# Performance work log

Measured on AMD Instinct MI355X. Metric: run time of the kernel, lower is better.

## Reference

```python
import jax, jax.numpy as jnp
import numpy as np

B, N, R, E = 4, 50000, 100000, 1_600_000   # batch, nodes (wavelets_col), wavelets_row, nnz
D_IN, H1, H2, D_OUT = 32, 32, 16, 1
NEG_SLOPE = 0.2


def _xavier(k, shape):
    lim = float(np.sqrt(6.0 / (shape[0] + shape[1])))
    return jax.random.uniform(k, shape, jnp.float32, -lim, lim)


def setup_inputs() -> dict:
    key = jax.random.key(0)
    ks = jax.random.split(key, 16)
    # wavelets: sparse (R x N); inverse wavelets: sparse (N x R)
    w_rows = jax.random.randint(ks[0], (E,), 0, R)
    w_cols = jax.random.randint(ks[1], (E,), 0, N)
    wi_rows = jax.random.randint(ks[2], (E,), 0, N)
    wi_cols = jax.random.randint(ks[3], (E,), 0, R)
    return {
        "wavelets_indices": jnp.stack([w_rows, w_cols]),
        "wavelets_values": jax.random.normal(ks[4], (E,), jnp.float32) * 0.05,
        "wavelets_inverse_indices": jnp.stack([wi_rows, wi_cols]),
        "wavelets_inverse_values": jax.random.normal(ks[5], (E,), jnp.float32) * 0.05,
        "x_features": jax.random.normal(ks[6], (B, N, D_IN), jnp.float32),
        "W1": _xavier(ks[7], (D_IN, H1)),
        "diag1": 0.9 + 0.2 * jax.random.uniform(ks[8], (R,), jnp.float32),
        "W2": _xavier(ks[9], (H1, H2)),
        "diag2": 0.9 + 0.2 * jax.random.uniform(ks[10], (R,), jnp.float32),
        "reg_co_w": _xavier(ks[11], (H2, D_OUT)),
        "reg_co_b": jnp.zeros((D_OUT,), jnp.float32),
        "reg_co2_w": _xavier(ks[12], (H2, D_OUT)),
        "reg_co2_b": jnp.zeros((D_OUT,), jnp.float32),
    }


def _gw_layer(x, W, diag, w_idx, w_val, wi_idx, wi_val):
    # filtered = X @ W  -> (B, N, d)
    h = jnp.einsum("bnd,de->bne", x, W)
    d = W.shape[1]
    # T = wavelets (R x N) @ h  : scatter-add of gathered edge messages
    msg = h[:, w_idx[1], :] * w_val[None, :, None]          # (B, E, d)
    t = jnp.zeros((x.shape[0], R, d), h.dtype).at[:, w_idx[0], :].add(msg)
    # out = (wavelets_inverse * diag) (N x R) @ T  (diag rescales columns)
    coef = wi_val * diag[wi_idx[1]]                         # (E,)
    msg2 = t[:, wi_idx[1], :] * coef[None, :, None]         # (B, E, d)
    out = jnp.zeros((x.shape[0], N, d), h.dtype).at[:, wi_idx[0], :].add(msg2)
    return jax.nn.leaky_relu(out, NEG_SLOPE)                # dropout p=0.0 -> identity


def reference(wavelets_indices, wavelets_values, wavelets_inverse_indices,
              wavelets_inverse_values, x_features, W1, diag1, W2, diag2,
              reg_co_w, reg_co_b, reg_co2_w, reg_co2_b):
    x = _gw_layer(x_features, W1, diag1, wavelets_indices, wavelets_values,
                  wavelets_inverse_indices, wavelets_inverse_values)
    x = _gw_layer(x, W2, diag2, wavelets_indices, wavelets_values,
                  wavelets_inverse_indices, wavelets_inverse_values)
    co = x[:, -2, :] @ reg_co_w + reg_co_b                  # (B, 1)
    co2 = x[:, -1, :] @ reg_co2_w + reg_co2_b               # (B, 1)
    return jnp.concatenate([co[:, None, :], co2[:, None, :]], axis=1)  # (B, 2, 1)
```

## Files before the change

### kernel.cpp

```cpp
#include <hip/hip_runtime.h>

#define NEG_SLOPE 0.2f

static const int B = 4, N = 50000, R = 100000, E = 1600000;
static const int X2_CAP = 4096;
static const int R2_CAP = 4096;
static const int N1_CAP = 4096;
static const int WDEG  = 64;
static const int WIDEG = 96;
static const int RBW = 3200;
static const int NBW = 1600;


__global__ void fusedA(const float* __restrict__ x, const float* __restrict__ W1,
                       float* __restrict__ h1,
                       const int4* __restrict__ wi_rows4, const int* __restrict__ wi_cols,
                       const float* __restrict__ wi_val,
                       unsigned* __restrict__ bitsR1, int2* __restrict__ x2list,
                       int* __restrict__ x2tail, int* __restrict__ r2list,
                       int* __restrict__ r2tail, int e4, int G1) {
    if ((int)blockIdx.x < G1) {
        __shared__ float sW[32 * 32];
        for (int i = threadIdx.x; i < 1024; i += blockDim.x) sW[i] = W1[i];
        __syncthreads();
        int id = blockIdx.x * blockDim.x + threadIdx.x;
        if (id >= N * B) return;
        int n = id >> 2, b = id & 3;
        const float* xr = x + ((size_t)b * N + n) * 32;
        float acc[32];
#pragma unroll
        for (int c = 0; c < 32; ++c) acc[c] = 0.f;
#pragma unroll
        for (int k = 0; k < 32; ++k) {
            float xv = xr[k];
#pragma unroll
            for (int c = 0; c < 32; ++c) acc[c] += xv * sW[k * 32 + c];
        }
        float* o = h1 + ((size_t)n * B + b) * 32;
#pragma unroll
        for (int c = 0; c < 32; ++c) o[c] = acc[c];
    } else {
        int blk = blockIdx.x - G1;
        int base = blk * (blockDim.x * 4) + threadIdx.x;
#pragma unroll
        for (int k = 0; k < 4; ++k) {
            int i = base + k * blockDim.x;
            if (i >= e4) continue;
            int4 r = wi_rows4[i];
            int rr[4] = {r.x, r.y, r.z, r.w};
#pragma unroll
            for (int j = 0; j < 4; ++j) {
                if (rr[j] >= N - 2) {
                    int ed = i * 4 + j;
                    int col = wi_cols[ed];
                    unsigned old = atomicOr(&bitsR1[col >> 5], 1u << (col & 31));
                    if (!((old >> (col & 31)) & 1u)) {
                        int p = atomicAdd(r2tail, 1);
                        if (p < R2_CAP) r2list[p] = col;
                    }
                    int pos = atomicAdd(x2tail, 1);
                    if (pos < X2_CAP)
                        x2list[pos] = make_int2(col * 2 + (rr[j] - (N - 2)),
                                                __float_as_int(wi_val[ed]));
                }
            }
        }
    }
}

__global__ void markB(const int4* __restrict__ w_rows4, const int* __restrict__ w_cols,
                      const unsigned* __restrict__ bitsR1, unsigned* __restrict__ bitsN1,
                      int* __restrict__ n1list, int* __restrict__ n1slot,
                      int* __restrict__ n1tail, int e4) {
    __shared__ int lcount, gbase;
    __shared__ int sbuf[1024];
    if (threadIdx.x == 0) lcount = 0;
    __syncthreads();
    int lane = threadIdx.x & 63;
    int i = blockIdx.x * blockDim.x + threadIdx.x;
    int4 r = make_int4(-1, -1, -1, -1);
    if (i < e4) r = w_rows4[i];
    int rr[4] = {r.x, r.y, r.z, r.w};
    unsigned fb[4];
#pragma unroll
    for (int j = 0; j < 4; ++j)
        fb[j] = (rr[j] >= 0) ? ((bitsR1[rr[j] >> 5] >> (rr[j] & 31)) & 1u) : 0u;
#pragma unroll
    for (int j = 0; j < 4; ++j) {
        bool isnew = false;
        int c = 0;
        if (fb[j]) {
            c = w_cols[i * 4 + j];
            unsigned old = atomicOr(&bitsN1[c >> 5], 1u << (c & 31));
            isnew = ((old >> (c & 31)) & 1u) == 0u;
        }
        unsigned long long m = __ballot(isnew);
        if (m) {
            int leader = __ffsll(m) - 1;
            int b0 = 0;
            if (lane == leader) b0 = atomicAdd(&lcount, __popcll(m));
            b0 = __shfl(b0, leader);
            if (isnew) sbuf[b0 + __popcll(m & ((1ull << lane) - 1))] = c;
        }
    }
    __syncthreads();
    if (threadIdx.x == 0) gbase = atomicAdd(n1tail, lcount);
    __syncthreads();
    for (int t = threadIdx.x; t < lcount; t += blockDim.x) {
        int n = sbuf[t];
        int slot = gbase + t;
        n1list[slot] = n;
        n1slot[n] = slot;
    }
}

__global__ void markC_wi(const int4* __restrict__ wi_rows4, const int* __restrict__ wi_cols,
                         const float* __restrict__ wi_val, const float* __restrict__ diag1,
                         const unsigned* __restrict__ bitsN1, const int* __restrict__ n1slot,
                         unsigned* __restrict__ bitsR2, int* __restrict__ wi_cnt,
                         int2* __restrict__ wi_pairsD,
                         int* __restrict__ r1list, int* __restrict__ r1tail, int e4) {
    __shared__ int lcount2, gbase2;
    __shared__ int r1buf[1024];
    if (threadIdx.x == 0) lcount2 = 0;
    __syncthreads();
    int lane = threadIdx.x & 63;
    int i = blockIdx.x * blockDim.x + threadIdx.x;
    int4 r = make_int4(-1, -1, -1, -1);
    if (i < e4) r = wi_rows4[i];
    int rr[4] = {r.x, r.y, r.z, r.w};
    unsigned fb[4];
#pragma unroll
    for (int j = 0; j < 4; ++j)
        fb[j] = (rr[j] >= 0) ? ((bitsN1[rr[j] >> 5] >> (rr[j] & 31)) & 1u) : 0u;
#pragma unroll
    for (int j = 0; j < 4; ++j) {
        bool isnew = false;
        int col = 0;
        if (fb[j]) {
            int ed = i * 4 + j;
            col = wi_cols[ed];
            float cf = wi_val[ed] * diag1[col];
            int slot = n1slot[rr[j]];
            int pos = atomicAdd(&wi_cnt[rr[j]], 1);
            if (slot < N1_CAP && pos < WIDEG)
                wi_pairsD[(size_t)slot * WIDEG + pos] =
                    make_int2(col, __float_as_int(cf));
            unsigned old = atomicOr(&bitsR2[col >> 5], 1u << (col & 31));
            isnew = ((old >> (col & 31)) & 1u) == 0u;
        }
        unsigned long long m2 = __ballot(isnew);
        if (m2) {
            int leader = __ffsll(m2) - 1;
            int b0 = 0;
            if (lane == leader) b0 = atomicAdd(&lcount2, __popcll(m2));
            b0 = __shfl(b0, leader);
            if (isnew)
                r1buf[b0 + __popcll(m2 & ((1ull << lane) - 1))] = col;
        }
    }
    __syncthreads();
    if (threadIdx.x == 0) gbase2 = atomicAdd(r1tail, lcount2);
    __syncthreads();
    for (int t = threadIdx.x; t < lcount2; t += blockDim.x) r1list[gbase2 + t] = r1buf[t];
}

__global__ void wplace(const int4* __restrict__ w_rows4, const int4* __restrict__ w_cols4,
                       const float4* __restrict__ w_val4,
                       const unsigned* __restrict__ bitsR1, const unsigned* __restrict__ bitsR2,
                       int* __restrict__ w_cnt, int2* __restrict__ w_pairsD, int e4) {
    int i = blockIdx.x * blockDim.x + threadIdx.x;
    if (i >= e4) return;
    int4 r = w_rows4[i];
    int4 c = w_cols4[i];
    float4 v = w_val4[i];
    int rr[4] = {r.x, r.y, r.z, r.w};
    int cc[4] = {c.x, c.y, c.z, c.w};
    float vv[4] = {v.x, v.y, v.z, v.w};
    unsigned fl[4];
#pragma unroll
    for (int j = 0; j < 4; ++j)
        fl[j] = ((bitsR1[rr[j] >> 5] | bitsR2[rr[j] >> 5]) >> (rr[j] & 31)) & 1u;
#pragma unroll
    for (int j = 0; j < 4; ++j) {
        if (fl[j]) {
            int pos = atomicAdd(&w_cnt[rr[j]], 1);
            if (pos < WDEG)
                w_pairsD[(size_t)rr[j] * WDEG + pos] =
                    make_int2(cc[j], __float_as_int(vv[j]));
        }
    }
}

__global__ void gather_t1(const float* __restrict__ h1, float* __restrict__ t1,
                          const int* __restrict__ w_cnt, const int2* __restrict__ w_pairsD,
                          const int* __restrict__ r1list, const int* __restrict__ r1tail) {
    int total = (*r1tail) * 32;
    int gstride = gridDim.x * blockDim.x;
    for (int idx = blockIdx.x * blockDim.x + threadIdx.x; idx < total; idx += gstride) {
        int row = r1list[idx >> 5];
        int rem = idx & 31;
        int c4 = rem & 7;
        int b = rem >> 3;
        int L = w_cnt[row]; if (L > WDEG) L = WDEG;
        const int2* pr = w_pairsD + (size_t)row * WDEG;
        const float4* sb = (const float4*)h1 + b * 8 + c4;
        float4 acc = make_float4(0.f, 0.f, 0.f, 0.f);
        int i = 0;
        int L4 = L & ~3;
        for (; i < L4; i += 4) {
            int2 p0 = pr[i + 0];
            int2 p1 = pr[i + 1];
            int2 p2 = pr[i + 2];
            int2 p3 = pr[i + 3];
            float4 s0 = sb[(size_t)p0.x * 32];
            float4 s1 = sb[(size_t)p1.x * 32];
            float4 s2 = sb[(size_t)p2.x * 32];
            float4 s3 = sb[(size_t)p3.x * 32];
            float v0 = __int_as_float(p0.y), v1 = __int_as_float(p1.y);
            float v2 = __int_as_float(p2.y), v3 = __int_as_float(p3.y);
            acc.x += v0 * s0.x + v1 * s1.x + v2 * s2.x + v3 * s3.x;
            acc.y += v0 * s0.y + v1 * s1.y + v2 * s2.y + v3 * s3.y;
            acc.z += v0 * s0.z + v1 * s1.z + v2 * s2.z + v3 * s3.z;
            acc.w += v0 * s0.w + v1 * s1.w + v2 * s2.w + v3 * s3.w;
        }
        for (; i < L; ++i) {
            int2 p = pr[i];
            float4 sv = sb[(size_t)p.x * 32];
            float v = __int_as_float(p.y);
            acc.x += v * sv.x; acc.y += v * sv.y; acc.z += v * sv.z; acc.w += v * sv.w;
        }
        ((float4*)t1)[(size_t)row * 32 + b * 8 + c4] = acc;
    }
}

__global__ void x1gemm2(const float* __restrict__ t1, const float* __restrict__ W2,
                        float* __restrict__ h2,
                        const int* __restrict__ n1list, const int* __restrict__ wi_cnt,
                        const int2* __restrict__ wi_pairsD,
                        const int* __restrict__ n1tail) {
    __shared__ float sW[32 * 16];
    __shared__ float xls[8][128];
    for (int i = threadIdx.x; i < 512; i += blockDim.x) sW[i] = W2[i];
    int n1c = *n1tail; if (n1c > N1_CAP) n1c = N1_CAP;
    int g = threadIdx.x >> 5;
    int t32 = threadIdx.x & 31;
    int b = t32 >> 3, c4 = t32 & 7;
    for (int base = blockIdx.x * 8; base < n1c; base += gridDim.x * 8) {
        int s = base + g;
        bool active = (s < n1c);
        int n = 0;
        if (active) {
            n = n1list[s];
            int L = wi_cnt[n]; if (L > WIDEG) L = WIDEG;
            const int2* pr = wi_pairsD + (size_t)s * WIDEG;
            const float4* sb = (const float4*)t1 + b * 8 + c4;
            float4 acc = make_float4(0.f, 0.f, 0.f, 0.f);
            int i = 0;
            int L2 = L & ~1;
            for (; i < L2; i += 2) {
                int2 p0 = pr[i + 0];
                int2 p1 = pr[i + 1];
                float4 s0 = sb[(size_t)p0.x * 32];
                float4 s1 = sb[(size_t)p1.x * 32];
                float v0 = __int_as_float(p0.y), v1 = __int_as_float(p1.y);
                acc.x += v0 * s0.x + v1 * s1.x;
                acc.y += v0 * s0.y + v1 * s1.y;
                acc.z += v0 * s0.z + v1 * s1.z;
                acc.w += v0 * s0.w + v1 * s1.w;
            }
            if (i < L) {
                int2 p = pr[i];
                float4 sv = sb[(size_t)p.x * 32];
                float v = __int_as_float(p.y);
                acc.x += v * sv.x; acc.y += v * sv.y; acc.z += v * sv.z; acc.w += v * sv.w;
            }
            float* xp = &xls[g][b * 32 + c4 * 4];
            xp[0] = acc.x > 0.f ? acc.x : NEG_SLOPE * acc.x;
            xp[1] = acc.y > 0.f ? acc.y : NEG_SLOPE * acc.y;
            xp[2] = acc.z > 0.f ? acc.z : NEG_SLOPE * acc.z;
            xp[3] = acc.w > 0.f ? acc.w : NEG_SLOPE * acc.w;
        }
        __syncthreads();
        if (active) {
#pragma unroll
            for (int half = 0; half < 2; ++half) {
                int o = t32 + half * 32;
                int bb = o >> 4, cc = o & 15;
                const float* xp = &xls[g][bb * 32];
                float acc = 0.f;
#pragma unroll
                for (int k = 0; k < 32; ++k) acc += xp[k] * sW[k * 16 + cc];
                h2[(size_t)n * 64 + o] = acc;
            }
        }
        __syncthreads();
    }
}

__global__ void t2x2heads(const float* __restrict__ h2,
                          const int* __restrict__ w_cnt, const int2* __restrict__ w_pairsD,
                          const int* __restrict__ r2list, const int* __restrict__ r2tail,
                          float* __restrict__ t2,
                          const int2* __restrict__ x2list, const int* __restrict__ x2tail,
                          const float* __restrict__ diag2,
                          const float* __restrict__ rw1, const float* __restrict__ rb1,
                          const float* __restrict__ rw2, const float* __restrict__ rb2,
                          float* __restrict__ out) {
    int r2c = *r2tail; if (r2c > R2_CAP) r2c = R2_CAP;
    for (int idx = threadIdx.x; idx < r2c * 16; idx += blockDim.x) {
        int row = r2list[idx >> 4];
        int rem = idx & 15;
        int c4 = rem & 3;
        int b = rem >> 2;
        int L = w_cnt[row]; if (L > WDEG) L = WDEG;
        const int2* pr = w_pairsD + (size_t)row * WDEG;
        const float4* sb = (const float4*)h2 + b * 4 + c4;
        float4 acc = make_float4(0.f, 0.f, 0.f, 0.f);
        for (int i = 0; i < L; ++i) {
            int2 p = pr[i];
            float4 sv = sb[(size_t)p.x * 16];
            float v = __int_as_float(p.y);
            acc.x += v * sv.x; acc.y += v * sv.y; acc.z += v * sv.z; acc.w += v * sv.w;
        }
        ((float4*)t2)[(size_t)row * 16 + b * 4 + c4] = acc;
    }
    __syncthreads();

    int cnt = *x2tail; if (cnt > X2_CAP) cnt = X2_CAP;
    int g = threadIdx.x >> 6, l = threadIdx.x & 63;
    int b = l >> 4, c = l & 15;
    float a0 = 0.f, a1 = 0.f;
    for (int i = g; i < cnt; i += 16) {
        int2 rec = x2list[i];
        int col = rec.x >> 1;
        float coef = __int_as_float(rec.y) * diag2[col];
        float v = t2[(size_t)col * 64 + b * 16 + c] * coef;
        if (rec.x & 1) a1 += v; else a0 += v;
    }
    __shared__ float red0[16][64], red1[16][64], xs[2][64];
    red0[g][l] = a0; red1[g][l] = a1;
    __syncthreads();
    if (threadIdx.x < 64) {
        float s0 = 0.f, s1 = 0.f;
#pragma unroll
        for (int gg = 0; gg < 16; ++gg) { s0 += red0[gg][l]; s1 += red1[gg][l]; }
        xs[0][l] = s0; xs[1][l] = s1;
    }
    __syncthreads();
    if (threadIdx.x < 8) {
        int bb = threadIdx.x >> 1, which = threadIdx.x & 1;
        const float* w = which ? rw2 : rw1;
        float acc = which ? rb2[0] : rb1[0];
        for (int k = 0; k < 16; ++k) {
            float xv = xs[which][bb * 16 + k];
            xv = xv > 0.f ? xv : NEG_SLOPE * xv;
            acc += xv * w[k];
        }
        out[bb * 2 + which] = acc;
    }
}

extern "C" void kernel_launch(void* const* d_in, const int* in_sizes, int n_in,
                              void* d_out, int out_size, void* d_ws, size_t ws_size,
                              hipStream_t stream) {
    const int*   w_rows  = (const int*)d_in[0];
    const int*   w_cols  = ((const int*)d_in[0]) + E;
    const float* w_val   = (const float*)d_in[1];
    const int*   wi_rows = (const int*)d_in[2];
    const int*   wi_cols = ((const int*)d_in[2]) + E;
    const float* wi_val  = (const float*)d_in[3];
    const float* x       = (const float*)d_in[4];
    const float* W1      = (const float*)d_in[5];
    const float* diag1   = (const float*)d_in[6];
    const float* W2      = (const float*)d_in[7];
    const float* diag2   = (const float*)d_in[8];
    const float* rw1     = (const float*)d_in[9];
    const float* rb1     = (const float*)d_in[10];
    const float* rw2     = (const float*)d_in[11];
    const float* rb2     = (const float*)d_in[12];
    float* out = (float*)d_out;

    float* h1 = (float*)d_ws;
    float* t1 = h1 + (size_t)B * N * 32;
    float* h2 = t1 + (size_t)B * R * 32;
    int* ip = (int*)(h2 + (size_t)B * N * 16);
    int* w_cnt  = ip; ip += R;
    int* wi_cnt = ip; ip += N;
    unsigned* bitsR1 = (unsigned*)ip; ip += RBW;
    unsigned* bitsR2 = (unsigned*)ip; ip += RBW;
    unsigned* bitsN1 = (unsigned*)ip; ip += NBW;
    int* tails  = ip; ip += 8;
    size_t zero_words = (size_t)(ip - w_cnt);
    int*  n1slot = ip; ip += N;
    int*  n1list = ip; ip += N;
    int*  r1list = ip; ip += R;
    int*  r2list = ip; ip += R2_CAP;
    int2* x2list = (int2*)ip; ip += 2 * X2_CAP;
    int2* w_pairsD  = (int2*)ip; ip += 2 * (size_t)R * WDEG;
    int2* wi_pairsD = (int2*)ip; ip += 2 * (size_t)N1_CAP * WIDEG;

    float* t2 = t1;

    const int blk = 256;
    const int e4 = E / 4;
    const int G1 = (N * B + blk - 1) / blk;
    const int G2 = (e4 + blk * 4 - 1) / (blk * 4);
    const int scanGrid = (e4 + blk - 1) / blk;

    (void)hipMemsetAsync(w_cnt, 0, zero_words * sizeof(int), stream);

    fusedA<<<G1 + G2, blk, 0, stream>>>(x, W1, h1, (const int4*)wi_rows, wi_cols, wi_val,
                                        bitsR1, x2list, tails + 0, r2list, tails + 1,
                                        e4, G1);
    markB<<<scanGrid, blk, 0, stream>>>((const int4*)w_rows, w_cols, bitsR1, bitsN1,
                                        n1list, n1slot, tails + 2, e4);
    markC_wi<<<scanGrid, blk, 0, stream>>>((const int4*)wi_rows, wi_cols, wi_val, diag1,
                                           bitsN1, n1slot, bitsR2, wi_cnt, wi_pairsD,
                                           r1list, tails + 3, e4);
    wplace<<<scanGrid, blk, 0, stream>>>((const int4*)w_rows, (const int4*)w_cols,
                                         (const float4*)w_val, bitsR1, bitsR2,
                                         w_cnt, w_pairsD, e4);
    gather_t1<<<4096, blk, 0, stream>>>(h1, t1, w_cnt, w_pairsD, r1list, tails + 3);
    x1gemm2<<<256, blk, 0, stream>>>(t1, W2, h2, n1list, wi_cnt, wi_pairsD, tails + 2);
    t2x2heads<<<1, 1024, 0, stream>>>(h2, w_cnt, w_pairsD, r2list, tails + 1,
                                      t2, x2list, tails + 0, diag2,
                                      rw1, rb1, rw2, rb2, out);
}
```

Measured before the change: 278.1 us.

## Fuse all phases into one cooperative persistent kernel with grid syncs

Replaces the memset and seven separate kernel launches with a single cooperative kernel that zeroes the workspace, then runs each marking, placement, gather and head phase separated by grid-wide syncs. The intent is to remove launch gaps and per-kernel ramp costs for a pipeline whose later phases touch only a small active subset. It also drops the full dense h1 = x@W1 product and fuses W1 into a later per-node stage, computing it only where needed. The cost is grid-sync overhead, fewer resident blocks looping over the edge arrays, and new 1024-entry per-block buffer caps that silently drop entries on overflow.

```diff
diff --git a/kernel.cpp b/kernel.cpp
--- a/kernel.cpp
+++ b/kernel.cpp
@@ -1,4 +1,7 @@
 #include <hip/hip_runtime.h>
+#include <hip/hip_cooperative_groups.h>
+
+namespace cg = cooperative_groups;
 
 #define NEG_SLOPE 0.2f
 
@@ -10,420 +13,421 @@
 static const int WIDEG = 96;
 static const int RBW = 3200;
 static const int NBW = 1600;
-
-
-__global__ void fusedA(const float* __restrict__ x, const float* __restrict__ W1,
-                       float* __restrict__ h1,
-                       const int4* __restrict__ wi_rows4, const int* __restrict__ wi_cols,
-                       const float* __restrict__ wi_val,
-                       unsigned* __restrict__ bitsR1, int2* __restrict__ x2list,
-                       int* __restrict__ x2tail, int* __restrict__ r2list,
-                       int* __restrict__ r2tail, int e4, int G1) {
-    if ((int)blockIdx.x < G1) {
-        __shared__ float sW[32 * 32];
-        for (int i = threadIdx.x; i < 1024; i += blockDim.x) sW[i] = W1[i];
+static const int ZWORDS = R + N + RBW + RBW + NBW + 8;
+
+struct KParams {
+    const int4*  w_rows4;  const int* w_cols;  const float* w_val;
+    const int4*  wi_rows4; const int* wi_cols; const float* wi_val;
+    const float* x;  const float* W1; const float* diag1;
+    const float* W2; const float* diag2;
+    const float* rw1; const float* rb1; const float* rw2; const float* rb2;
+    float* out;
+    float* t1;
+    float* h2;
+    int* w_cnt; int* wi_cnt;
+    unsigned* bitsR1; unsigned* bitsR2; unsigned* bitsN1;
+    int* tails;
+    int* n1slot; int* n1list; int* r1list; int* r2list;
+    int2* x2list; int2* w_pairsD; int2* wi_pairsD;
+    int e4;
+};
+
+union SMem {
+    struct { int lcount; int gbase; int buf[1024]; } comp;
+    struct { float W1s[1024]; float W2s[512];
+             float uls[8][128]; float x1ls[8][128]; } p6;
+    struct { float red0[4][64]; float red1[4][64]; float xs[2][64]; } p8;
+};
+
+__global__ void __launch_bounds__(256, 4) fused(KParams P) {
+    cg::grid_group grid = cg::this_grid();
+    const int tid  = threadIdx.x;
+    const int gtid = blockIdx.x * blockDim.x + tid;
+    const int T    = gridDim.x * blockDim.x;
+    const int lane = tid & 63;
+    __shared__ SMem sm;
+
+    for (int i = gtid; i < ZWORDS; i += T) P.w_cnt[i] = 0;
+    grid.sync();
+
+    for (int i = gtid; i < P.e4; i += T) {
+        int4 r = P.wi_rows4[i];
+        int rr[4] = {r.x, r.y, r.z, r.w};
+#pragma unroll
+        for (int j = 0; j < 4; ++j) {
+            if (rr[j] >= N - 2) {
+                int ed = i * 4 + j;
+                int col = P.wi_cols[ed];
+                unsigned old = atomicOr(&P.bitsR1[col >> 5], 1u << (col & 31));
+                if (!((old >> (col & 31)) & 1u)) {
+                    int p = atomicAdd(&P.tails[1], 1);
+                    if (p < R2_CAP) P.r2list[p] = col;
+                }
+                int pos = atomicAdd(&P.tails[0], 1);
+                if (pos < X2_CAP)
+                    P.x2list[pos] = make_int2(col * 2 + (rr[j] - (N - 2)),
+                                              __float_as_int(P.wi_val[ed]));
+            }
+        }
+    }
+    grid.sync();
+
+    if (tid == 0) sm.comp.lcount = 0;
+    __syncthreads();
+    {
+        int niter = (P.e4 + T - 1) / T;
+        for (int it = 0; it < niter; ++it) {
+            int i = it * T + gtid;
+            int4 r = make_int4(-1, -1, -1, -1);
+            if (i < P.e4) r = P.w_rows4[i];
+            int rr[4] = {r.x, r.y, r.z, r.w};
+            unsigned fb[4];
+#pragma unroll
+            for (int j = 0; j < 4; ++j)
+                fb[j] = (rr[j] >= 0) ? ((P.bitsR1[rr[j] >> 5] >> (rr[j] & 31)) & 1u) : 0u;
+#pragma unroll
+            for (int j = 0; j < 4; ++j) {
+                bool isnew = false;
+                int c = 0;
+                if (fb[j]) {
+                    c = P.w_cols[i * 4 + j];
+                    unsigned old = atomicOr(&P.bitsN1[c >> 5], 1u << (c & 31));
+                    isnew = ((old >> (c & 31)) & 1u) == 0u;
+                }
+                unsigned long long m = __ballot(isnew);
+                if (m) {
+                    int leader = __ffsll(m) - 1;
+                    int b0 = 0;
+                    if (lane == leader) b0 = atomicAdd(&sm.comp.lcount, __popcll(m));
+                    b0 = __shfl(b0, leader);
+                    if (isnew) {
+                        int p = b0 + __popcll(m & ((1ull << lane) - 1));
+                        if (p < 1024) sm.comp.buf[p] = c;
+                    }
+                }
+            }
+        }
+    }
+    __syncthreads();
+    {
+        int lc = sm.comp.lcount; if (lc > 1024) lc = 1024;
+        if (tid == 0) sm.comp.gbase = atomicAdd(&P.tails[2], lc);
         __syncthreads();
-        int id = blockIdx.x * blockDim.x + threadIdx.x;
-        if (id >= N * B) return;
-        int n = id >> 2, b = id & 3;
-        const float* xr = x + ((size_t)b * N + n) * 32;
-        float acc[32];
-#pragma unroll
-        for (int c = 0; c < 32; ++c) acc[c] = 0.f;
-#pragma unroll
-        for (int k = 0; k < 32; ++k) {
-            float xv = xr[k];
-#pragma unroll
-            for (int c = 0; c < 32; ++c) acc[c] += xv * sW[k * 32 + c];
-        }
-        float* o = h1 + ((size_t)n * B + b) * 32;
-#pragma unroll
-        for (int c = 0; c < 32; ++c) o[c] = acc[c];
-    } else {
-        int blk = blockIdx.x - G1;
-        int base = blk * (blockDim.x * 4) + threadIdx.x;
-#pragma unroll
-        for (int k = 0; k < 4; ++k) {
-            int i = base + k * blockDim.x;
-            if (i >= e4) continue;
-            int4 r = wi_rows4[i];
+        for (int t = tid; t < lc; t += 256) {
+            int n = sm.comp.buf[t];
+            int slot = sm.comp.gbase + t;
+            if (slot < N1_CAP) { P.n1list[slot] = n; P.n1slot[n] = slot; }
+        }
+    }
+    grid.sync();
+
+    if (tid == 0) sm.comp.lcount = 0;
+    __syncthreads();
+    {
+        int niter = (P.e4 + T - 1) / T;
+        for (int it = 0; it < niter; ++it) {
+            int i = it * T + gtid;
+            int4 r = make_int4(-1, -1, -1, -1);
+            if (i < P.e4) r = P.wi_rows4[i];
             int rr[4] = {r.x, r.y, r.z, r.w};
+            unsigned fb[4];
+#pragma unroll
+            for (int j = 0; j < 4; ++j)
+                fb[j] = (rr[j] >= 0) ? ((P.bitsN1[rr[j] >> 5] >> (rr[j] & 31)) & 1u) : 0u;
 #pragma unroll
             for (int j = 0; j < 4; ++j) {
-                if (rr[j] >= N - 2) {
+                bool isnew = false;
+                int col = 0;
+                if (fb[j]) {
                     int ed = i * 4 + j;
-                    int col = wi_cols[ed];
-                    unsigned old = atomicOr(&bitsR1[col >> 5], 1u << (col & 31));
-                    if (!((old >> (col & 31)) & 1u)) {
-                        int p = atomicAdd(r2tail, 1);
-                        if (p < R2_CAP) r2list[p] = col;
+                    col = P.wi_cols[ed];
+                    float cf = P.wi_val[ed] * P.diag1[col];
+                    int slot = P.n1slot[rr[j]];
+                    int pos = atomicAdd(&P.wi_cnt[rr[j]], 1);
+                    if (slot < N1_CAP && pos < WIDEG)
+                        P.wi_pairsD[(size_t)slot * WIDEG + pos] =
+                            make_int2(col, __float_as_int(cf));
+                    unsigned old = atomicOr(&P.bitsR2[col >> 5], 1u << (col & 31));
+                    isnew = ((old >> (col & 31)) & 1u) == 0u;
+                }
+                unsigned long long m2 = __ballot(isnew);
+                if (m2) {
+                    int leader = __ffsll(m2) - 1;
+                    int b0 = 0;
+                    if (lane == leader) b0 = atomicAdd(&sm.comp.lcount, __popcll(m2));
+                    b0 = __shfl(b0, leader);
+                    if (isnew) {
+                        int p = b0 + __popcll(m2 & ((1ull << lane) - 1));
+                        if (p < 1024) sm.comp.buf[p] = col;
                     }
-                    int pos = atomicAdd(x2tail, 1);
-                    if (pos < X2_CAP)
-                        x2list[pos] = make_int2(col * 2 + (rr[j] - (N - 2)),
-                                                __float_as_int(wi_val[ed]));
-                }
-            }
-        }
-    }
-}
-
-__global__ void markB(const int4* __restrict__ w_rows4, const int* __restrict__ w_cols,
-                      const unsigned* __restrict__ bitsR1, unsigned* __restrict__ bitsN1,
-                      int* __restrict__ n1list, int* __restrict__ n1slot,
-                      int* __restrict__ n1tail, int e4) {
-    __shared__ int lcount, gbase;
-    __shared__ int sbuf[1024];
-    if (threadIdx.x == 0) lcount = 0;
+                }
+            }
+        }
+    }
     __syncthreads();
-    int lane = threadIdx.x & 63;
-    int i = blockIdx.x * blockDim.x + threadIdx.x;
-    int4 r = make_int4(-1, -1, -1, -1);
-    if (i < e4) r = w_rows4[i];
-    int rr[4] = {r.x, r.y, r.z, r.w};
-    unsigned fb[4];
-#pragma unroll
-    for (int j = 0; j < 4; ++j)
-        fb[j] = (rr[j] >= 0) ? ((bitsR1[rr[j] >> 5] >> (rr[j] & 31)) & 1u) : 0u;
-#pragma unroll
-    for (int j = 0; j < 4; ++j) {
-        bool isnew = false;
-        int c = 0;
-        if (fb[j]) {
-            c = w_cols[i * 4 + j];
-            unsigned old = atomicOr(&bitsN1[c >> 5], 1u << (c & 31));
-            isnew = ((old >> (c & 31)) & 1u) == 0u;
-        }
-        unsigned long long m = __ballot(isnew);
-        if (m) {
-            int leader = __ffsll(m) - 1;
-            int b0 = 0;
-            if (lane == leader) b0 = atomicAdd(&lcount, __popcll(m));
-            b0 = __shfl(b0, leader);
-            if (isnew) sbuf[b0 + __popcll(m & ((1ull << lane) - 1))] = c;
-        }
-    }
-    __syncthreads();
-    if (threadIdx.x == 0) gbase = atomicAdd(n1tail, lcount);
-    __syncthreads();
-    for (int t = threadIdx.x; t < lcount; t += blockDim.x) {
-        int n = sbuf[t];
-        int slot = gbase + t;
-        n1list[slot] = n;
-        n1slot[n] = slot;
-    }
-}
-
-__global__ void markC_wi(const int4* __restrict__ wi_rows4, const int* __restrict__ wi_cols,
-                         const float* __restrict__ wi_val, const float* __restrict__ diag1,
-                         const unsigned* __restrict__ bitsN1, const int* __restrict__ n1slot,
-                         unsigned* __restrict__ bitsR2, int* __restrict__ wi_cnt,
-                         int2* __restrict__ wi_pairsD,
-                         int* __restrict__ r1list, int* __restrict__ r1tail, int e4) {
-    __shared__ int lcount2, gbase2;
-    __shared__ int r1buf[1024];
-    if (threadIdx.x == 0) lcount2 = 0;
-    __syncthreads();
-    int lane = threadIdx.x & 63;
-    int i = blockIdx.x * blockDim.x + threadIdx.x;
-    int4 r = make_int4(-1, -1, -1, -1);
-    if (i < e4) r = wi_rows4[i];
-    int rr[4] = {r.x, r.y, r.z, r.w};
-    unsigned fb[4];
-#pragma unroll
-    for (int j = 0; j < 4; ++j)
-        fb[j] = (rr[j] >= 0) ? ((bitsN1[rr[j] >> 5] >> (rr[j] & 31)) & 1u) : 0u;
-#pragma unroll
-    for (int j = 0; j < 4; ++j) {
-        bool isnew = false;
-        int col = 0;
-        if (fb[j]) {
-            int ed = i * 4 + j;
-            col = wi_cols[ed];
-            float cf = wi_val[ed] * diag1[col];
-            int slot = n1slot[rr[j]];
-            int pos = atomicAdd(&wi_cnt[rr[j]], 1);
-            if (slot < N1_CAP && pos < WIDEG)
-                wi_pairsD[(size_t)slot * WIDEG + pos] =
-                    make_int2(col, __float_as_int(cf));
-            unsigned old = atomicOr(&bitsR2[col >> 5], 1u << (col & 31));
-            isnew = ((old >> (col & 31)) & 1u) == 0u;
-        }
-        unsigned long long m2 = __ballot(isnew);
-        if (m2) {
-            int leader = __ffsll(m2) - 1;
-            int b0 = 0;
-            if (lane == leader) b0 = atomicAdd(&lcount2, __popcll(m2));
-            b0 = __shfl(b0, leader);
-            if (isnew)
-                r1buf[b0 + __popcll(m2 & ((1ull << lane) - 1))] = col;
-        }
-    }
-    __syncthreads();
-    if (threadIdx.x == 0) gbase2 = atomicAdd(r1tail, lcount2);
-    __syncthreads();
-    for (int t = threadIdx.x; t < lcount2; t += blockDim.x) r1list[gbase2 + t] = r1buf[t];
-}
-
-__global__ void wplace(const int4* __restrict__ w_rows4, const int4* __restrict__ w_cols4,
-                       const float4* __restrict__ w_val4,
-                       const unsigned* __restrict__ bitsR1, const unsigned* __restrict__ bitsR2,
-                       int* __restrict__ w_cnt, int2* __restrict__ w_pairsD, int e4) {
-    int i = blockIdx.x * blockDim.x + threadIdx.x;
-    if (i >= e4) return;
-    int4 r = w_rows4[i];
-    int4 c = w_cols4[i];
-    float4 v = w_val4[i];
-    int rr[4] = {r.x, r.y, r.z, r.w};
-    int cc[4] = {c.x, c.y, c.z, c.w};
-    float vv[4] = {v.x, v.y, v.z, v.w};
-    unsigned fl[4];
-#pragma unroll
-    for (int j = 0; j < 4; ++j)
-        fl[j] = ((bitsR1[rr[j] >> 5] | bitsR2[rr[j] >> 5]) >> (rr[j] & 31)) & 1u;
-#pragma unroll
-    for (int j = 0; j < 4; ++j) {
-        if (fl[j]) {
-            int pos = atomicAdd(&w_cnt[rr[j]], 1);
-            if (pos < WDEG)
-                w_pairsD[(size_t)rr[j] * WDEG + pos] =
-                    make_int2(cc[j], __float_as_int(vv[j]));
-        }
-    }
-}
-
-__global__ void gather_t1(const float* __restrict__ h1, float* __restrict__ t1,
-                          const int* __restrict__ w_cnt, const int2* __restrict__ w_pairsD,
-                          const int* __restrict__ r1list, const int* __restrict__ r1tail) {
-    int total = (*r1tail) * 32;
-    int gstride = gridDim.x * blockDim.x;
-    for (int idx = blockIdx.x * blockDim.x + threadIdx.x; idx < total; idx += gstride) {
-        int row = r1list[idx >> 5];
-        int rem = idx & 31;
-        int c4 = rem & 7;
-        int b = rem >> 3;
-        int L = w_cnt[row]; if (L > WDEG) L = WDEG;
-        const int2* pr = w_pairsD + (size_t)row * WDEG;
-        const float4* sb = (const float4*)h1 + b * 8 + c4;
-        float4 acc = make_float4(0.f, 0.f, 0.f, 0.f);
-        int i = 0;
-        int L4 = L & ~3;
-        for (; i < L4; i += 4) {
-            int2 p0 = pr[i + 0];
-            int2 p1 = pr[i + 1];
-            int2 p2 = pr[i + 2];
-            int2 p3 = pr[i + 3];
-            float4 s0 = sb[(size_t)p0.x * 32];
-            float4 s1 = sb[(size_t)p1.x * 32];
-            float4 s2 = sb[(size_t)p2.x * 32];
-            float4 s3 = sb[(size_t)p3.x * 32];
-            float v0 = __int_as_float(p0.y), v1 = __int_as_float(p1.y);
-            float v2 = __int_as_float(p2.y), v3 = __int_as_float(p3.y);
-            acc.x += v0 * s0.x + v1 * s1.x + v2 * s2.x + v3 * s3.x;
-            acc.y += v0 * s0.y + v1 * s1.y + v2 * s2.y + v3 * s3.y;
-            acc.z += v0 * s0.z + v1 * s1.z + v2 * s2.z + v3 * s3.z;
-            acc.w += v0 * s0.w + v1 * s1.w + v2 * s2.w + v3 * s3.w;
-        }
-        for (; i < L; ++i) {
-            int2 p = pr[i];
-            float4 sv = sb[(size_t)p.x * 32];
-            float v = __int_as_float(p.y);
-            acc.x += v * sv.x; acc.y += v * sv.y; acc.z += v * sv.z; acc.w += v * sv.w;
-        }
-        ((float4*)t1)[(size_t)row * 32 + b * 8 + c4] = acc;
-    }
-}
-
-__global__ void x1gemm2(const float* __restrict__ t1, const float* __restrict__ W2,
-                        float* __restrict__ h2,
-                        const int* __restrict__ n1list, const int* __restrict__ wi_cnt,
-                        const int2* __restrict__ wi_pairsD,
-                        const int* __restrict__ n1tail) {
-    __shared__ float sW[32 * 16];
-    __shared__ float xls[8][128];
-    for (int i = threadIdx.x; i < 512; i += blockDim.x) sW[i] = W2[i];
-    int n1c = *n1tail; if (n1c > N1_CAP) n1c = N1_CAP;
-    int g = threadIdx.x >> 5;
-    int t32 = threadIdx.x & 31;
-    int b = t32 >> 3, c4 = t32 & 7;
-    for (int base = blockIdx.x * 8; base < n1c; base += gridDim.x * 8) {
-        int s = base + g;
-        bool active = (s < n1c);
-        int n = 0;
-        if (active) {
-            n = n1list[s];
-            int L = wi_cnt[n]; if (L > WIDEG) L = WIDEG;
-            const int2* pr = wi_pairsD + (size_t)s * WIDEG;
-            const float4* sb = (const float4*)t1 + b * 8 + c4;
+    {
+        int lc = sm.comp.lcount; if (lc > 1024) lc = 1024;
+        if (tid == 0) sm.comp.gbase = atomicAdd(&P.tails[3], lc);
+        __syncthreads();
+        for (int t = tid; t < lc; t += 256) P.r1list[sm.comp.gbase + t] = sm.comp.buf[t];
+    }
+    grid.sync();
+
+    {
+        const int4* wc4 = (const int4*)P.w_cols;
+        const float4* wv4 = (const float4*)P.w_val;
+        for (int i = gtid; i < P.e4; i += T) {
+            int4 r = P.w_rows4[i];
+            int4 c = wc4[i];
+            float4 v = wv4[i];
+            int rr[4] = {r.x, r.y, r.z, r.w};
+            int cc[4] = {c.x, c.y, c.z, c.w};
+            float vv[4] = {v.x, v.y, v.z, v.w};
+            unsigned fl[4];
+#pragma unroll
+            for (int j = 0; j < 4; ++j)
+                fl[j] = ((P.bitsR1[rr[j] >> 5] | P.bitsR2[rr[j] >> 5]) >> (rr[j] & 31)) & 1u;
+            int pos[4];
+#pragma unroll
+            for (int j = 0; j < 4; ++j)
+                pos[j] = fl[j] ? atomicAdd(&P.w_cnt[rr[j]], 1) : WDEG;
+#pragma unroll
+            for (int j = 0; j < 4; ++j)
+                if (pos[j] < WDEG)
+                    P.w_pairsD[(size_t)rr[j] * WDEG + pos[j]] =
+                        make_int2(cc[j], __float_as_int(vv[j]));
+        }
+    }
+    grid.sync();
+
+    {
+        int r1c = P.tails[3];
+        int total = r1c * 32;
+        for (int idx = gtid; idx < total; idx += T) {
+            int row = P.r1list[idx >> 5];
+            int rem = idx & 31;
+            int c4 = rem & 7;
+            int b = rem >> 3;
+            int L = P.w_cnt[row]; if (L > WDEG) L = WDEG;
+            const int2* pr = P.w_pairsD + (size_t)row * WDEG;
+            const float4* sb = (const float4*)P.x + (size_t)b * N * 8 + c4;
             float4 acc = make_float4(0.f, 0.f, 0.f, 0.f);
             int i = 0;
-            int L2 = L & ~1;
-            for (; i < L2; i += 2) {
+            int L4 = L & ~3;
+            for (; i < L4; i += 4) {
                 int2 p0 = pr[i + 0];
                 int2 p1 = pr[i + 1];
-                float4 s0 = sb[(size_t)p0.x * 32];
-                float4 s1 = sb[(size_t)p1.x * 32];
+                int2 p2 = pr[i + 2];
+                int2 p3 = pr[i + 3];
+                float4 s0 = sb[(size_t)p0.x * 8];
+                float4 s1 = sb[(size_t)p1.x * 8];
+                float4 s2 = sb[(size_t)p2.x * 8];
+                float4 s3 = sb[(size_t)p3.x * 8];
                 float v0 = __int_as_float(p0.y), v1 = __int_as_float(p1.y);
-                acc.x += v0 * s0.x + v1 * s1.x;
-                acc.y += v0 * s0.y + v1 * s1.y;
-                acc.z += v0 * s0.z + v1 * s1.z;
-                acc.w += v0 * s0.w + v1 * s1.w;
-            }
-            if (i < L) {
+                float v2 = __int_as_float(p2.y), v3 = __int_as_float(p3.y);
+                acc.x += v0 * s0.x + v1 * s1.x + v2 * s2.x + v3 * s3.x;
+                acc.y += v0 * s0.y + v1 * s1.y + v2 * s2.y + v3 * s3.y;
+                acc.z += v0 * s0.z + v1 * s1.z + v2 * s2.z + v3 * s3.z;
+                acc.w += v0 * s0.w + v1 * s1.w + v2 * s2.w + v3 * s3.w;
+            }
+            for (; i < L; ++i) {
                 int2 p = pr[i];
-                float4 sv = sb[(size_t)p.x * 32];
+                float4 sv = sb[(size_t)p.x * 8];
                 float v = __int_as_float(p.y);
                 acc.x += v * sv.x; acc.y += v * sv.y; acc.z += v * sv.z; acc.w += v * sv.w;
             }
-            float* xp = &xls[g][b * 32 + c4 * 4];
-            xp[0] = acc.x > 0.f ? acc.x : NEG_SLOPE * acc.x;
-            xp[1] = acc.y > 0.f ? acc.y : NEG_SLOPE * acc.y;
-            xp[2] = acc.z > 0.f ? acc.z : NEG_SLOPE * acc.z;
-            xp[3] = acc.w > 0.f ? acc.w : NEG_SLOPE * acc.w;
-        }
+            ((float4*)P.t1)[(size_t)row * 32 + b * 8 + c4] = acc;
+        }
+    }
+    grid.sync();
+
+    {
+        for (int i = tid; i < 1024; i += 256) sm.p6.W1s[i] = P.W1[i];
+        for (int i = tid; i < 512; i += 256) sm.p6.W2s[i] = P.W2[i];
         __syncthreads();
-        if (active) {
-#pragma unroll
-            for (int half = 0; half < 2; ++half) {
-                int o = t32 + half * 32;
-                int bb = o >> 4, cc = o & 15;
-                const float* xp = &xls[g][bb * 32];
-                float acc = 0.f;
-#pragma unroll
-                for (int k = 0; k < 32; ++k) acc += xp[k] * sW[k * 16 + cc];
-                h2[(size_t)n * 64 + o] = acc;
-            }
-        }
+        int n1c = P.tails[2]; if (n1c > N1_CAP) n1c = N1_CAP;
+        int g = tid >> 5;
+        int t32 = tid & 31;
+        int b = t32 >> 3, c4 = t32 & 7;
+        for (int base = blockIdx.x * 8; base < n1c; base += gridDim.x * 8) {
+            int s = base + g;
+            bool active = (s < n1c);
+            int n = 0;
+            if (active) {
+                n = P.n1list[s];
+                int L = P.wi_cnt[n]; if (L > WIDEG) L = WIDEG;
+                const int2* pr = P.wi_pairsD + (size_t)s * WIDEG;
+                const float4* sb = (const float4*)P.t1 + b * 8 + c4;
+                float4 acc = make_float4(0.f, 0.f, 0.f, 0.f);
+                int i = 0;
+                int L2 = L & ~1;
+                for (; i < L2; i += 2) {
+                    int2 p0 = pr[i + 0];
+                    int2 p1 = pr[i + 1];
+                    float4 s0 = sb[(size_t)p0.x * 32];
+                    float4 s1 = sb[(size_t)p1.x * 32];
+                    float v0 = __int_as_float(p0.y), v1 = __int_as_float(p1.y);
+                    acc.x += v0 * s0.x + v1 * s1.x;
+                    acc.y += v0 * s0.y + v1 * s1.y;
+                    acc.z += v0 * s0.z + v1 * s1.z;
+                    acc.w += v0 * s0.w + v1 * s1.w;
+                }
+                if (i < L) {
+                    int2 p = pr[i];
+                    float4 sv = sb[(size_t)p.x * 32];
+                    float v = __int_as_float(p.y);
+                    acc.x += v * sv.x; acc.y += v * sv.y; acc.z += v * sv.z; acc.w += v * sv.w;
+                }
+                float* up = &sm.p6.uls[g][b * 32 + c4 * 4];
+                up[0] = acc.x; up[1] = acc.y; up[2] = acc.z; up[3] = acc.w;
+            }
+            __syncthreads();
+            if (active) {
+                const float* urow = &sm.p6.uls[g][b * 32];
+                float o0 = 0.f, o1 = 0.f, o2 = 0.f, o3 = 0.f;
+#pragma unroll
+                for (int k = 0; k < 32; ++k) {
+                    float uk = urow[k];
+                    const float* wr = &sm.p6.W1s[k * 32 + c4 * 4];
+                    o0 += uk * wr[0]; o1 += uk * wr[1]; o2 += uk * wr[2]; o3 += uk * wr[3];
+                }
+                float* xp = &sm.p6.x1ls[g][b * 32 + c4 * 4];
+                xp[0] = o0 > 0.f ? o0 : NEG_SLOPE * o0;
+                xp[1] = o1 > 0.f ? o1 : NEG_SLOPE * o1;
+                xp[2] = o2 > 0.f ? o2 : NEG_SLOPE * o2;
+                xp[3] = o3 > 0.f ? o3 : NEG_SLOPE * o3;
+            }
+            __syncthreads();
+            if (active) {
+#pragma unroll
+                for (int half = 0; half < 2; ++half) {
+                    int o = t32 + half * 32;
+                    int bb = o >> 4, cc = o & 15;
+                    const float* xp = &sm.p6.x1ls[g][bb * 32];
+                    float acc = 0.f;
+#pragma unroll
+                    for (int k = 0; k < 32; ++k) acc += xp[k] * sm.p6.W2s[k * 16 + cc];
+                    P.h2[(size_t)n * 64 + o] = acc;
+                }
+            }
+            __syncthreads();
+        }
+    }
+    grid.sync();
+
+    if (blockIdx.x != 0) return;
+    {
+        int r2c = P.tails[1]; if (r2c > R2_CAP) r2c = R2_CAP;
+        for (int idx = tid; idx < r2c * 16; idx += 256) {
+            int row = P.r2list[idx >> 4];
+            int rem = idx & 15;
+            int c4 = rem & 3;
+            int b = rem >> 2;
+            int L = P.w_cnt[row]; if (L > WDEG) L = WDEG;
+            const int2* pr = P.w_pairsD + (size_t)row * WDEG;
+            const float4* sb = (const float4*)P.h2 + b * 4 + c4;
+            float4 acc = make_float4(0.f, 0.f, 0.f, 0.f);
+            for (int i = 0; i < L; ++i) {
+                int2 p = pr[i];
+                float4 sv = sb[(size_t)p.x * 16];
+                float v = __int_as_float(p.y);
+                acc.x += v * sv.x; acc.y += v * sv.y; acc.z += v * sv.z; acc.w += v * sv.w;
+            }
+            ((float4*)P.t1)[(size_t)row * 16 + b * 4 + c4] = acc;
+        }
+    }
+    __syncthreads();
+    {
+        int cnt = P.tails[0]; if (cnt > X2_CAP) cnt = X2_CAP;
+        int g2 = tid >> 6, l = tid & 63;
+        int b = l >> 4, c = l & 15;
+        float a0 = 0.f, a1 = 0.f;
+        for (int i = g2; i < cnt; i += 4) {
+            int2 rec = P.x2list[i];
+            int col = rec.x >> 1;
+            float coef = __int_as_float(rec.y) * P.diag2[col];
+            float v = P.t1[(size_t)col * 64 + b * 16 + c] * coef;
+            if (rec.x & 1) a1 += v; else a0 += v;
+        }
+        sm.p8.red0[g2][l] = a0; sm.p8.red1[g2][l] = a1;
         __syncthreads();
-    }
-}
-
-__global__ void t2x2heads(const float* __restrict__ h2,
-                          const int* __restrict__ w_cnt, const int2* __restrict__ w_pairsD,
-                          const int* __restrict__ r2list, const int* __restrict__ r2tail,
-                          float* __restrict__ t2,
-                          const int2* __restrict__ x2list, const int* __restrict__ x2tail,
-                          const float* __restrict__ diag2,
-                          const float* __restrict__ rw1, const float* __restrict__ rb1,
-                          const float* __restrict__ rw2, const float* __restrict__ rb2,
-                          float* __restrict__ out) {
-    int r2c = *r2tail; if (r2c > R2_CAP) r2c = R2_CAP;
-    for (int idx = threadIdx.x; idx < r2c * 16; idx += blockDim.x) {
-        int row = r2list[idx >> 4];
-        int rem = idx & 15;
-        int c4 = rem & 3;
-        int b = rem >> 2;
-        int L = w_cnt[row]; if (L > WDEG) L = WDEG;
-        const int2* pr = w_pairsD + (size_t)row * WDEG;
-        const float4* sb = (const float4*)h2 + b * 4 + c4;
-        float4 acc = make_float4(0.f, 0.f, 0.f, 0.f);
-        for (int i = 0; i < L; ++i) {
-            int2 p = pr[i];
-            float4 sv = sb[(size_t)p.x * 16];
-            float v = __int_as_float(p.y);
-            acc.x += v * sv.x; acc.y += v * sv.y; acc.z += v * sv.z; acc.w += v * sv.w;
-        }
-        ((float4*)t2)[(size_t)row * 16 + b * 4 + c4] = acc;
-    }
-    __syncthreads();
-
-    int cnt = *x2tail; if (cnt > X2_CAP) cnt = X2_CAP;
-    int g = threadIdx.x >> 6, l = threadIdx.x & 63;
-    int b = l >> 4, c = l & 15;
-    float a0 = 0.f, a1 = 0.f;
-    for (int i = g; i < cnt; i += 16) {
-        int2 rec = x2list[i];
-        int col = rec.x >> 1;
-        float coef = __int_as_float(rec.y) * diag2[col];
-        float v = t2[(size_t)col * 64 + b * 16 + c] * coef;
-        if (rec.x & 1) a1 += v; else a0 += v;
-    }
-    __shared__ float red0[16][64], red1[16][64], xs[2][64];
-    red0[g][l] = a0; red1[g][l] = a1;
-    __syncthreads();
-    if (threadIdx.x < 64) {
-        float s0 = 0.f, s1 = 0.f;
-#pragma unroll
-        for (int gg = 0; gg < 16; ++gg) { s0 += red0[gg][l]; s1 += red1[gg][l]; }
-        xs[0][l] = s0; xs[1][l] = s1;
-    }
-    __syncthreads();
-    if (threadIdx.x < 8) {
-        int bb = threadIdx.x >> 1, which = threadIdx.x & 1;
-        const float* w = which ? rw2 : rw1;
-        float acc = which ? rb2[0] : rb1[0];
-        for (int k = 0; k < 16; ++k) {
-            float xv = xs[which][bb * 16 + k];
-            xv = xv > 0.f ? xv : NEG_SLOPE * xv;
-            acc += xv * w[k];
-        }
-        out[bb * 2 + which] = acc;
+        if (tid < 64) {
+            float s0 = 0.f, s1 = 0.f;
+#pragma unroll
+            for (int gg = 0; gg < 4; ++gg) { s0 += sm.p8.red0[gg][tid]; s1 += sm.p8.red1[gg][tid]; }
+            sm.p8.xs[0][tid] = s0; sm.p8.xs[1][tid] = s1;
+        }
+        __syncthreads();
+        if (tid < 8) {
+            int bb = tid >> 1, which = tid & 1;
+            const float* w = which ? P.rw2 : P.rw1;
+            float acc = which ? P.rb2[0] : P.rb1[0];
+            for (int k = 0; k < 16; ++k) {
+                float xv = sm.p8.xs[which][bb * 16 + k];
+                xv = xv > 0.f ? xv : NEG_SLOPE * xv;
+                acc += xv * w[k];
+            }
+            P.out[bb * 2 + which] = acc;
+        }
     }
 }
 
 extern "C" void kernel_launch(void* const* d_in, const int* in_sizes, int n_in,
                               void* d_out, int out_size, void* d_ws, size_t ws_size,
                               hipStream_t stream) {
-    const int*   w_rows  = (const int*)d_in[0];
-    const int*   w_cols  = ((const int*)d_in[0]) + E;
-    const float* w_val   = (const float*)d_in[1];
-    const int*   wi_rows = (const int*)d_in[2];
-    const int*   wi_cols = ((const int*)d_in[2]) + E;
-    const float* wi_val  = (const float*)d_in[3];
-    const float* x       = (const float*)d_in[4];
-    const float* W1      = (const float*)d_in[5];
-    const float* diag1   = (const float*)d_in[6];
-    const float* W2      = (const float*)d_in[7];
-    const float* diag2   = (const float*)d_in[8];
-    const float* rw1     = (const float*)d_in[9];
-    const float* rb1     = (const float*)d_in[10];
-    const float* rw2     = (const float*)d_in[11];
-    const float* rb2     = (const float*)d_in[12];
-    float* out = (float*)d_out;
-
-    float* h1 = (float*)d_ws;
-    float* t1 = h1 + (size_t)B * N * 32;
+    KParams P;
+    P.w_rows4  = (const int4*)d_in[0];
+    P.w_cols   = ((const int*)d_in[0]) + E;
+    P.w_val    = (const float*)d_in[1];
+    P.wi_rows4 = (const int4*)d_in[2];
+    P.wi_cols  = ((const int*)d_in[2]) + E;
+    P.wi_val   = (const float*)d_in[3];
+    P.x        = (const float*)d_in[4];
+    P.W1       = (const float*)d_in[5];
+    P.diag1    = (const float*)d_in[6];
+    P.W2       = (const float*)d_in[7];
+    P.diag2    = (const float*)d_in[8];
+    P.rw1      = (const float*)d_in[9];
+    P.rb1      = (const float*)d_in[10];
+    P.rw2      = (const float*)d_in[11];
+    P.rb2      = (const float*)d_in[12];
+    P.out      = (float*)d_out;
+
+    float* t1 = (float*)d_ws;
     float* h2 = t1 + (size_t)B * R * 32;
     int* ip = (int*)(h2 + (size_t)B * N * 16);
-    int* w_cnt  = ip; ip += R;
-    int* wi_cnt = ip; ip += N;
-    unsigned* bitsR1 = (unsigned*)ip; ip += RBW;
-    unsigned* bitsR2 = (unsigned*)ip; ip += RBW;
-    unsigned* bitsN1 = (unsigned*)ip; ip += NBW;
-    int* tails  = ip; ip += 8;
-    size_t zero_words = (size_t)(ip - w_cnt);
-    int*  n1slot = ip; ip += N;
-    int*  n1list = ip; ip += N;
-    int*  r1list = ip; ip += R;
-    int*  r2list = ip; ip += R2_CAP;
-    int2* x2list = (int2*)ip; ip += 2 * X2_CAP;
-    int2* w_pairsD  = (int2*)ip; ip += 2 * (size_t)R * WDEG;
-    int2* wi_pairsD = (int2*)ip; ip += 2 * (size_t)N1_CAP * WIDEG;
-
-    float* t2 = t1;
-
-    const int blk = 256;
-    const int e4 = E / 4;
-    const int G1 = (N * B + blk - 1) / blk;
-    const int G2 = (e4 + blk * 4 - 1) / (blk * 4);
-    const int scanGrid = (e4 + blk - 1) / blk;
-
-    (void)hipMemsetAsync(w_cnt, 0, zero_words * sizeof(int), stream);
-
-    fusedA<<<G1 + G2, blk, 0, stream>>>(x, W1, h1, (const int4*)wi_rows, wi_cols, wi_val,
-                                        bitsR1, x2list, tails + 0, r2list, tails + 1,
-                                        e4, G1);
-    markB<<<scanGrid, blk, 0, stream>>>((const int4*)w_rows, w_cols, bitsR1, bitsN1,
-                                        n1list, n1slot, tails + 2, e4);
-    markC_wi<<<scanGrid, blk, 0, stream>>>((const int4*)wi_rows, wi_cols, wi_val, diag1,
-                                           bitsN1, n1slot, bitsR2, wi_cnt, wi_pairsD,
-                                           r1list, tails + 3, e4);
-    wplace<<<scanGrid, blk, 0, stream>>>((const int4*)w_rows, (const int4*)w_cols,
-                                         (const float4*)w_val, bitsR1, bitsR2,
-                                         w_cnt, w_pairsD, e4);
-    gather_t1<<<4096, blk, 0, stream>>>(h1, t1, w_cnt, w_pairsD, r1list, tails + 3);
-    x1gemm2<<<256, blk, 0, stream>>>(t1, W2, h2, n1list, wi_cnt, wi_pairsD, tails + 2);
-    t2x2heads<<<1, 1024, 0, stream>>>(h2, w_cnt, w_pairsD, r2list, tails + 1,
-                                      t2, x2list, tails + 0, diag2,
-                                      rw1, rb1, rw2, rb2, out);
+    P.w_cnt  = ip; ip += R;
+    P.wi_cnt = ip; ip += N;
+    P.bitsR1 = (unsigned*)ip; ip += RBW;
+    P.bitsR2 = (unsigned*)ip; ip += RBW;
+    P.bitsN1 = (unsigned*)ip; ip += NBW;
+    P.tails  = ip; ip += 8;
+    P.n1slot = ip; ip += N;
+    P.n1list = ip; ip += N;
+    P.r1list = ip; ip += R;
+    P.r2list = ip; ip += R2_CAP;
+    P.x2list = (int2*)ip; ip += 2 * X2_CAP;
+    P.w_pairsD  = (int2*)ip; ip += 2 * (size_t)R * WDEG;
+    P.wi_pairsD = (int2*)ip; ip += 2 * (size_t)N1_CAP * WIDEG;
+    P.t1 = t1;
+    P.h2 = h2;
+    P.e4 = E / 4;
+
+    static int gridsz = 0;
+    if (gridsz == 0) {
+        int dev = 0;
+        (void)hipGetDevice(&dev);
+        hipDeviceProp_t prop;
+        (void)hipGetDeviceProperties(&prop, dev);
+        int maxb = 0;
+        (void)hipOccupancyMaxActiveBlocksPerMultiprocessor(&maxb, fused, 256, 0);
+        if (maxb < 1) maxb = 1;
+        long g = (long)prop.multiProcessorCount * maxb;
+        if (g > 2048) g = 2048;
+        if (g < 1) g = 1;
+        gridsz = (int)g;
+    }
+
+    void* args[] = { &P };
+    (void)hipLaunchCooperativeKernel(fused, dim3(gridsz), dim3(256), args, 0, stream);
 }
```

Measured after the change: 694.4 us. +149.7%, slower.
